# Kernel tuning notes

Hardware: AMD Instinct MI355X
Metric: run time of the kernel (lower is better)

Reference implementation:

```python
import jax, jax.numpy as jnp
import numpy as np

B, C, H, W = 8, 64, 112, 112
F, KH, KW = 128, 3, 3
SPARSITY = 0.7  # fraction of kernel entries zeroed (Uniform connector)


def setup_inputs() -> dict:
    key = jax.random.key(0)
    k1, k2, k3 = jax.random.split(key, 3)
    inputs = jax.random.normal(k1, (B, C, H, W), dtype=jnp.float32)
    fan_in = C * KH * KW
    limit = float(np.sqrt(6.0 / (F + fan_in)))
    vals = jax.random.uniform(k2, (F, fan_in), minval=-limit, maxval=limit, dtype=jnp.float32)
    mask = (jax.random.uniform(k3, (F, fan_in)) >= SPARSITY).astype(jnp.float32)
    kernel = vals * mask  # dense representation of the sparse kernel
    return {"inputs": inputs, "kernel": kernel}


def _extract_patches(x, kh, kw):
    # x: [B, S1, S2, C]; VALID padding, stride 1, rate 1.
    # Matches tf.image.extract_patches depth ordering: (pi, pj) major, channel minor.
    Bb, S1, S2, Cc = x.shape
    o1, o2 = S1 - kh + 1, S2 - kw + 1
    pats = jnp.stack(
        [x[:, i:i + o1, j:j + o2, :] for i in range(kh) for j in range(kw)],
        axis=3,
    )  # [B, o1, o2, kh*kw, C]
    return pats.reshape(Bb, o1, o2, kh * kw * Cc)


def reference(inputs, kernel):
    # inputs: [B, C, H, W] (NCHW, per bias_add data_format and build())
    x = jnp.transpose(inputs, (0, 3, 2, 1))  # [B, W, H, C] (perm [0,3,2,1] in original)
    p = _extract_patches(x, KH, KW)          # [B, oW, oH, KH*KW*C]
    # spmm(kernel [F, K], im2col [K, B*oW*oH]) expressed as a single contraction
    out = jnp.einsum('bwhk,fk->bfwh', p, kernel)  # [B, F, oW, oH]
    return out
```

## Files before the change

### kernel.cpp

```cpp
#include <hip/hip_runtime.h>

typedef unsigned short u16;
typedef unsigned int u32;
typedef _Float16 f16x8 __attribute__((ext_vector_type(8)));
typedef float f32x16 __attribute__((ext_vector_type(16)));

#define B_ 8
#define C_ 64
#define H_ 112
#define W_ 112
#define HW_ 12544
#define F_ 128
#define OH_ 110
#define OW_ 110
#define OWOH 12100
#define NPOS 96800
#define KK_ 576
#define NT_ 384
#define NWGQ 1012
#define OCTSTRIDE 802816
#define AELEMS 73728
#define AQUAR 18432

__device__ __forceinline__ void gl_lds16(const void* g, void* l) {
  __builtin_amdgcn_global_load_lds((const __attribute__((address_space(1))) void*)g,
                                   (__attribute__((address_space(3))) void*)l,
                                   16, 0, 0);
}

__global__ __launch_bounds__(256) void prep_all(const float* __restrict__ in,
                                                const float* __restrict__ k,
                                                u16* __restrict__ xT,
                                                u16* __restrict__ kT) {
  const int bid = blockIdx.x;
  const int tid = threadIdx.x;
  if (bid >= 896) {
    const int base = (bid - 896) * 2048;
#pragma unroll
    for (int t = 0; t < 8; ++t) {
      int idx = base + t * 256 + tid;
      int c = idx & 7;
      int f = (idx >> 3) & 127;
      int hf = (idx >> 10) & 1;
      int ko16 = idx >> 11;
      _Float16 h = (_Float16)k[f * KK_ + ko16 * 16 + hf * 8 + c];
      kT[idx] = __builtin_bit_cast(u16, h);
    }
    return;
  }
  __shared__ float tile[8][8][113];
  const int b = bid / 112;
  const int r = bid % 112;
  const int oct = r / 14;
  const int hs = (r % 14) * 8;

  for (int idx = tid; idx < 8 * 8 * 112; idx += 256) {
    int c = idx / 896;
    int rem = idx - c * 896;
    int h = rem / 112;
    int w = rem - h * 112;
    tile[c][h][w] = in[(((size_t)(b * 64 + oct * 8 + c)) * 112 + (hs + h)) * 112 + w];
  }
  __syncthreads();

  for (int idx = tid; idx < 896; idx += 256) {
    int w = idx >> 3;
    int h = idx & 7;
    f16x8 v;
#pragma unroll
    for (int c = 0; c < 8; ++c) v[c] = (_Float16)tile[c][h][w];
    size_t o = ((((size_t)oct * B_ + b) * W_ + w) * H_ + (hs + h)) * 8;
    *(f16x8*)(xT + o) = v;
  }
}

__global__ __launch_bounds__(256, 4) void conv_mfma(
    const u16* __restrict__ xT, const u16* __restrict__ kT,
    float* __restrict__ out) {
  __shared__ u16 lds[AQUAR];

  const int tid = threadIdx.x;
  const int wave = tid >> 6;
  const int lane = tid & 63;
  const int l31 = lane & 31;
  const int hi = lane >> 5;

  const int orig = blockIdx.x;
  const int xcd = orig & 7;
  const int sub = orig >> 3;
  const int work = (xcd < 4 ? xcd * 127 : 508 + (xcd - 4) * 126) + sub;
  const int nblk = work >> 2;
  const int fq = work & 3;
  const int n0 = nblk * NT_ + wave * 96;

  int posOff[3];
#pragma unroll
  for (int ni = 0; ni < 3; ++ni) {
    int n = n0 + ni * 32 + l31;
    if (n >= NPOS) n = 0;
    int b = n / OWOH;
    int r = n - b * OWOH;
    int w = r / OH_;
    int h = r - w * OH_;
    posOff[ni] = ((b * W_ + w) * H_ + h) * 8;
  }

#pragma unroll
  for (int it = 0; it < 9; ++it) {
    const int m = it * 256 + tid;
    const int src = ((m >> 5) << 7) + (fq << 5) + (m & 31);
    gl_lds16(kT + src * 8, (char*)lds + m * 16);
  }
  __syncthreads();

  f32x16 acc[3] = {};

#pragma unroll
  for (int s = 0; s < 18; ++s) {
    const int tap = s >> 1;
    const int half = s & 1;
    const int i = tap / 3;
    const int j = tap - i * 3;
    const int sShift = (i * H_ + j) * 8;

    f16x8 bh[6];
#pragma unroll
    for (int ni = 0; ni < 3; ++ni)
#pragma unroll
      for (int t = 0; t < 2; ++t)
        bh[ni * 2 + t] = *(const f16x8*)(xT + (half * 4 + t * 2 + hi) * OCTSTRIDE +
                                         posOff[ni] + sShift);

    f16x8 ah[2];
#pragma unroll
    for (int t = 0; t < 2; ++t)
      ah[t] = *(const f16x8*)&lds[((((s * 2 + t) * 2 + hi) << 5) + l31) * 8];

#pragma unroll
    for (int t = 0; t < 2; ++t)
#pragma unroll
      for (int ni = 0; ni < 3; ++ni)
        acc[ni] = __builtin_amdgcn_mfma_f32_32x32x16_f16(ah[t], bh[ni * 2 + t], acc[ni], 0, 0, 0);
  }

#pragma unroll
  for (int ni = 0; ni < 3; ++ni) {
    int n = n0 + ni * 32 + l31;
    if (n >= NPOS) continue;
    int b = n / OWOH;
    int r = n - b * OWOH;
    int w = r / OH_;
    int h = r - w * OH_;
    float* op = out + ((size_t)(b * F_) * OW_ + w) * OH_ + h;
    const int fbase = fq * 32 + 4 * hi;
#pragma unroll
    for (int reg = 0; reg < 16; ++reg) {
      int f = fbase + (reg & 3) + 8 * (reg >> 2);
      op[(size_t)f * OWOH] = acc[ni][reg];
    }
  }
}

__global__ void naive_conv(const float* __restrict__ in, const float* __restrict__ ker,
                           float* __restrict__ out) {
  int idx = blockIdx.x * 256 + threadIdx.x;
  const int total = B_ * F_ * OW_ * OH_;
  if (idx >= total) return;
  int h = idx % OH_;
  int w = (idx / OH_) % OW_;
  int f = (idx / (OW_ * OH_)) % F_;
  int b = idx / (F_ * OW_ * OH_);
  float s = 0.f;
  for (int tap = 0; tap < 9; ++tap) {
    int i = tap / 3, j = tap % 3;
    const float* ip = in + ((size_t)b * C_ * H_ + (h + j)) * W_ + (w + i);
    const float* kp = ker + (size_t)f * KK_ + tap * C_;
    for (int c = 0; c < C_; ++c) s += ip[(size_t)c * HW_] * kp[c];
  }
  out[idx] = s;
}

extern "C" void kernel_launch(void* const* d_in, const int* in_sizes, int n_in,
                              void* d_out, int out_size, void* d_ws, size_t ws_size,
                              hipStream_t stream) {
  const float* in = (const float*)d_in[0];
  const float* ker = (const float*)d_in[1];
  float* out = (float*)d_out;

  const size_t xElems = (size_t)B_ * H_ * W_ * C_;
  const size_t need = (xElems + AELEMS) * 2;

  if (ws_size < need) {
    int total = B_ * F_ * OW_ * OH_;
    naive_conv<<<(total + 255) / 256, 256, 0, stream>>>(in, ker, out);
    return;
  }

  u16* xT = (u16*)d_ws;
  u16* kT = xT + xElems;

  prep_all<<<932, 256, 0, stream>>>(in, ker, xT, kT);
  conv_mfma<<<NWGQ, 256, 0, stream>>>(xT, kT, out);
}
```

Baseline: 42.37 us.

## Widen conv tile to 64 filters per workgroup, staging kernel in two halves

Each workgroup now covers 64 output filters instead of 32, so twice as many MFMAs reuse each loaded B (input patch) fragment. This halves the grid and the redundant global reads of the transposed input. To keep LDS the same size, the filter slice is staged in two K-halves with an extra barrier between them. Accumulator registers double and occupancy drops from 4 to 3 waves per SIMD, which may reduce latency hiding.

```diff
diff --git a/kernel.cpp b/kernel.cpp
--- a/kernel.cpp
+++ b/kernel.cpp
@@ -17,10 +17,10 @@
 #define NPOS 96800
 #define KK_ 576
 #define NT_ 384
-#define NWGQ 1012
+#define NWGF 506
 #define OCTSTRIDE 802816
 #define AELEMS 73728
-#define AQUAR 18432
+#define AKHALF 18432
 
 __device__ __forceinline__ void gl_lds16(const void* g, void* l) {
   __builtin_amdgcn_global_load_lds((const __attribute__((address_space(1))) void*)g,
@@ -74,10 +74,10 @@
   }
 }
 
-__global__ __launch_bounds__(256, 4) void conv_mfma(
+__global__ __launch_bounds__(256, 3) void conv_mfma(
     const u16* __restrict__ xT, const u16* __restrict__ kT,
     float* __restrict__ out) {
-  __shared__ u16 lds[AQUAR];
+  __shared__ u16 lds[AKHALF];
 
   const int tid = threadIdx.x;
   const int wave = tid >> 6;
@@ -88,9 +88,9 @@
   const int orig = blockIdx.x;
   const int xcd = orig & 7;
   const int sub = orig >> 3;
-  const int work = (xcd < 4 ? xcd * 127 : 508 + (xcd - 4) * 126) + sub;
-  const int nblk = work >> 2;
-  const int fq = work & 3;
+  const int wg = (xcd < 2 ? xcd * 64 : 128 + (xcd - 2) * 63) + sub;
+  const int nblk = wg >> 1;
+  const int fh = wg & 1;
   const int n0 = nblk * NT_ + wave * 96;
 
   int posOff[3];
@@ -105,43 +105,51 @@
     posOff[ni] = ((b * W_ + w) * H_ + h) * 8;
   }
 
-#pragma unroll
-  for (int it = 0; it < 9; ++it) {
-    const int m = it * 256 + tid;
-    const int src = ((m >> 5) << 7) + (fq << 5) + (m & 31);
-    gl_lds16(kT + src * 8, (char*)lds + m * 16);
-  }
-  __syncthreads();
-
-  f32x16 acc[3] = {};
-
-#pragma unroll
-  for (int s = 0; s < 18; ++s) {
-    const int tap = s >> 1;
-    const int half = s & 1;
-    const int i = tap / 3;
-    const int j = tap - i * 3;
-    const int sShift = (i * H_ + j) * 8;
-
-    f16x8 bh[6];
-#pragma unroll
-    for (int ni = 0; ni < 3; ++ni)
-#pragma unroll
-      for (int t = 0; t < 2; ++t)
-        bh[ni * 2 + t] = *(const f16x8*)(xT + (half * 4 + t * 2 + hi) * OCTSTRIDE +
-                                         posOff[ni] + sShift);
-
-    f16x8 ah[2];
-#pragma unroll
-    for (int t = 0; t < 2; ++t)
-      ah[t] = *(const f16x8*)&lds[((((s * 2 + t) * 2 + hi) << 5) + l31) * 8];
-
-#pragma unroll
-    for (int t = 0; t < 2; ++t)
-#pragma unroll
-      for (int ni = 0; ni < 3; ++ni)
-        acc[ni] = __builtin_amdgcn_mfma_f32_32x32x16_f16(ah[t], bh[ni * 2 + t], acc[ni], 0, 0, 0);
-  }
+  auto stageA = [&](int half) {
+#pragma unroll
+    for (int it = 0; it < 9; ++it) {
+      const int m = it * 256 + tid;
+      const int src = (((m >> 6) + half * 36) << 7) + (fh << 6) + (m & 63);
+      gl_lds16(kT + src * 8, (char*)lds + m * 16);
+    }
+  };
+
+  f32x16 acc[2][3] = {};
+
+#define STEP(S, HALFBUF)                                                                 \
+  {                                                                                      \
+    const int tap = (S) >> 1;                                                            \
+    const int bhalf = (S)&1;                                                             \
+    const int i_ = tap / 3, j_ = tap - i_ * 3;                                           \
+    const int sShift = (i_ * H_ + j_) * 8;                                               \
+    f16x8 bh[6];                                                                         \
+    _Pragma("unroll") for (int ni = 0; ni < 3; ++ni)                                     \
+        _Pragma("unroll") for (int t = 0; t < 2; ++t)                                    \
+            bh[ni * 2 + t] = *(const f16x8*)(xT + (bhalf * 4 + t * 2 + hi) * OCTSTRIDE + \
+                                             posOff[ni] + sShift);                       \
+    f16x8 ah[4];                                                                         \
+    const int sl = (S)-9 * (HALFBUF);                                                    \
+    _Pragma("unroll") for (int t = 0; t < 2; ++t)                                        \
+        _Pragma("unroll") for (int mi = 0; mi < 2; ++mi)                                 \
+            ah[t * 2 + mi] =                                                             \
+                *(const f16x8*)&lds[((((sl * 2 + t) * 2 + hi) << 6) + mi * 32 + l31) * 8]; \
+    _Pragma("unroll") for (int t = 0; t < 2; ++t)                                        \
+        _Pragma("unroll") for (int mi = 0; mi < 2; ++mi)                                 \
+            _Pragma("unroll") for (int ni = 0; ni < 3; ++ni)                             \
+                acc[mi][ni] = __builtin_amdgcn_mfma_f32_32x32x16_f16(                    \
+                    ah[t * 2 + mi], bh[ni * 2 + t], acc[mi][ni], 0, 0, 0);               \
+  }
+
+  stageA(0);
+  __syncthreads();
+  STEP(0, 0) STEP(1, 0) STEP(2, 0) STEP(3, 0) STEP(4, 0)
+  STEP(5, 0) STEP(6, 0) STEP(7, 0) STEP(8, 0)
+  __syncthreads();
+  stageA(1);
+  __syncthreads();
+  STEP(9, 1) STEP(10, 1) STEP(11, 1) STEP(12, 1) STEP(13, 1)
+  STEP(14, 1) STEP(15, 1) STEP(16, 1) STEP(17, 1)
+#undef STEP
 
 #pragma unroll
   for (int ni = 0; ni < 3; ++ni) {
@@ -152,11 +160,14 @@
     int w = r / OH_;
     int h = r - w * OH_;
     float* op = out + ((size_t)(b * F_) * OW_ + w) * OH_ + h;
-    const int fbase = fq * 32 + 4 * hi;
-#pragma unroll
-    for (int reg = 0; reg < 16; ++reg) {
-      int f = fbase + (reg & 3) + 8 * (reg >> 2);
-      op[(size_t)f * OWOH] = acc[ni][reg];
+#pragma unroll
+    for (int mi = 0; mi < 2; ++mi) {
+      const int fbase = fh * 64 + mi * 32 + 4 * hi;
+#pragma unroll
+      for (int reg = 0; reg < 16; ++reg) {
+        int f = fbase + (reg & 3) + 8 * (reg >> 2);
+        op[(size_t)f * OWOH] = acc[mi][ni][reg];
+      }
     }
   }
 }
@@ -200,5 +211,5 @@
   u16* kT = xT + xElems;
 
   prep_all<<<932, 256, 0, stream>>>(in, ker, xT, kT);
-  conv_mfma<<<NWGQ, 256, 0, stream>>>(xT, kT, out);
-}
+  conv_mfma<<<NWGF, 256, 0, stream>>>(xT, kT, out);
+}
```

After: 40.41 us. 1.05x faster.
